# Optimization experiments

Hardware: AMD Instinct MI355X
Metric: run time of the kernel (lower is better)

## Reference

```python
import jax, jax.numpy as jnp
import numpy as np

H, KVH, HD, DM = 32, 8, 128, 4096  # attention heads, kv heads, head_dim, hidden


def _rope_tables(batch, seq, head_dim):
    # standard RoPE tables, flattened per token to match varlen layout
    inv_freq = 1.0 / (10000.0 ** (np.arange(0, head_dim, 2, dtype=np.float32) / head_dim))
    pos = np.arange(seq, dtype=np.float32)
    freqs = np.outer(pos, inv_freq)                      # [S, HD/2]
    emb = np.concatenate([freqs, freqs], axis=-1)        # [S, HD]
    cos = np.tile(np.cos(emb), (batch, 1))               # [B*S, HD]
    sin = np.tile(np.sin(emb), (batch, 1))
    return jnp.asarray(cos), jnp.asarray(sin)


def setup_inputs() -> dict:
    key = jax.random.key(0)
    k1, k2 = jax.random.split(key)
    B, S = 2, 1024
    hidden_states = jax.random.normal(k1, (B * S, DM), dtype=jnp.float32) * 0.02
    w_qkv = jax.random.normal(k2, (DM, (H + 2 * KVH) * HD), dtype=jnp.float32) * 0.02
    cos, sin = _rope_tables(B, S, HD)
    return {"hidden_states": hidden_states, "w_qkv": w_qkv, "cos": cos,
            "sin": sin, "batch_size": B, "seq_len": S}


def _rotate_half(x):
    half = x.shape[-1] // 2
    return jnp.concatenate([-x[..., half:], x[..., :half]], axis=-1)


def reference(hidden_states, w_qkv, cos, sin, batch_size, seq_len):
    B, S = batch_size, seq_len
    T = B * S
    n_rep = H // KVH
    scale = 1.0 / jnp.sqrt(jnp.asarray(HD, hidden_states.dtype))

    qkv = hidden_states @ w_qkv                           # [T, (H+2*KVH)*HD]
    q = qkv[:, : H * HD].reshape(T, H, HD)
    k = qkv[:, H * HD : (H + KVH) * HD].reshape(T, KVH, HD)
    v = qkv[:, (H + KVH) * HD :].reshape(T, KVH, HD)

    # RoPE (rotary half) on q and k
    c, s = cos[:, None, :], sin[:, None, :]
    q = q * c + _rotate_half(q) * s
    k = k * c + _rotate_half(k) * s

    # prefill SDPA branch: reshape to [B, heads, S, HD], GQA repeat on kv heads
    q = q.reshape(B, S, H, HD).transpose(0, 2, 1, 3)      # [B,H,S,HD]
    k = k.reshape(B, S, KVH, HD).transpose(0, 2, 1, 3)
    v = v.reshape(B, S, KVH, HD).transpose(0, 2, 1, 3)
    k = jnp.repeat(k, n_rep, axis=1)                      # [B,H,S,HD]
    v = jnp.repeat(v, n_rep, axis=1)

    scores = jnp.einsum("bhqd,bhkd->bhqk", q, k) * scale  # [B,H,S,S]
    causal = jnp.tril(jnp.ones((S, S), dtype=bool))
    scores = jnp.where(causal, scores, jnp.asarray(-jnp.inf, scores.dtype))
    probs = jax.nn.softmax(scores, axis=-1)
    attn = jnp.einsum("bhqk,bhkd->bhqd", probs, v)        # [B,H,S,HD]

    # postprocess_attention_output: transpose back and flatten tokens
    attn = attn.transpose(0, 2, 1, 3).reshape(T, H * HD)  # [T, H*HD]
    return attn
```

## Files before the change

kernel.cpp:

```cpp
#include <hip/hip_runtime.h>
#include <hip/hip_bf16.h>
#include <stdint.h>

constexpr int NH   = 32;
constexpr int NKVH = 8;
constexpr int HD   = 128;
constexpr int DM   = 4096;
constexpr int B    = 2;
constexpr int S    = 1024;
constexpr int T    = B * S;
constexpr int QKVN = (NH + 2 * NKVH) * HD;
constexpr int KOFF = NH * HD;
constexpr int VOFF = (NH + NKVH) * HD;

typedef float floatx4 __attribute__((ext_vector_type(4)));
typedef floatx4 floatx4_a __attribute__((may_alias));
typedef __bf16 bf16x8 __attribute__((ext_vector_type(8)));
typedef bf16x8 bf16x8_a __attribute__((may_alias));
typedef __bf16 bf16_a __attribute__((may_alias));

__device__ __forceinline__ void gload_lds16(const void* g, void* l) {
  __builtin_amdgcn_global_load_lds(
      (const __attribute__((address_space(1))) void*)g,
      (__attribute__((address_space(3))) void*)l, 16, 0, 0);
}

__global__ __launch_bounds__(256) void convert_a(const float* __restrict__ A,
                                                 __bf16* __restrict__ A16) {
  const size_t i = (size_t)(blockIdx.x * 256 + threadIdx.x) * 8;
  floatx4 v0 = *(const floatx4_a*)(A + i);
  floatx4 v1 = *(const floatx4_a*)(A + i + 4);
  bf16x8 o;
#pragma unroll
  for (int e = 0; e < 4; ++e) {
    o[e] = (__bf16)v0[e];
    o[e + 4] = (__bf16)v1[e];
  }
  *(bf16x8_a*)(A16 + i) = o;
}

__global__ __launch_bounds__(256) void transpose_w(
    const float* __restrict__ W, __bf16* __restrict__ WT) {
  __shared__ __align__(16) __bf16 ls[64][72];
  const int k0 = blockIdx.x * 64;
  const int n0 = blockIdx.y * 64;
  const int tx = threadIdx.x & 15, ty = threadIdx.x >> 4;
#pragma unroll
  for (int rr = 0; rr < 4; ++rr) {
    const int k = ty + rr * 16;
    floatx4 v = *(const floatx4_a*)(W + (size_t)(k0 + k) * QKVN + n0 + tx * 4);
#pragma unroll
    for (int e = 0; e < 4; ++e) ls[tx * 4 + e][k] = (__bf16)v[e];
  }
  __syncthreads();
#pragma unroll
  for (int it = 0; it < 2; ++it) {
    const int n = (threadIdx.x >> 3) + it * 32;
    const int c = threadIdx.x & 7;
    bf16x8 o = *(const bf16x8_a*)(&ls[n][c * 8]);
    *(bf16x8_a*)(WT + (size_t)(n0 + n) * DM + k0 + c * 8) = o;
  }
}

__global__ __launch_bounds__(256) void gemm_mfma(
    const __bf16* __restrict__ A16, const __bf16* __restrict__ W16T,
    float* __restrict__ C) {
  __shared__ __align__(16) __bf16 Asig[128 * 64];
  __shared__ __align__(16) __bf16 Bsig[128 * 64];

  const int tid = threadIdx.x;
  const int lane = tid & 63, w = tid >> 6;
  const int l15 = lane & 15, g = lane >> 4;
  const int r7 = l15 & 7;
  const int m0 = blockIdx.x * 128;
  const int n0 = blockIdx.y * 128;
  const int wrbase = (w >> 1) * 64, wcbase = (w & 1) * 64;

  const int srow = tid >> 3;
  const int sce = ((tid & 7) ^ (srow & 7)) << 3;
  const __bf16* agp = A16 + (size_t)(m0 + srow) * DM + sce;
  const __bf16* bgp = W16T + (size_t)(n0 + srow) * DM + sce;
  char* al = (char*)Asig + w * 1024;
  char* bl = (char*)Bsig + w * 1024;

  const char* Abase = (const char*)Asig + (wrbase + l15) * 128;
  const char* Bbase = (const char*)Bsig + (wcbase + l15) * 128;

  floatx4 acc[4][4];
#pragma unroll
  for (int i = 0; i < 4; ++i)
#pragma unroll
    for (int j = 0; j < 4; ++j) acc[i][j] = (floatx4){0.f, 0.f, 0.f, 0.f};

  for (int kk = 0; kk < DM; kk += 64) {
    __syncthreads();
#pragma unroll
    for (int j = 0; j < 4; ++j) {
      gload_lds16(agp + kk + (size_t)(32 * j) * DM, al + j * 4096);
      gload_lds16(bgp + kk + (size_t)(32 * j) * DM, bl + j * 4096);
    }
    __syncthreads();

#pragma unroll
    for (int kh = 0; kh < 2; ++kh) {
      const int sw = (((kh << 2) | g) ^ r7) << 4;
      bf16x8 af[4], bf[4];
#pragma unroll
      for (int i = 0; i < 4; ++i) {
        af[i] = *(const bf16x8_a*)(Abase + i * 2048 + sw);
        bf[i] = *(const bf16x8_a*)(Bbase + i * 2048 + sw);
      }
#pragma unroll
      for (int i = 0; i < 4; ++i)
#pragma unroll
        for (int j = 0; j < 4; ++j)
          acc[i][j] = __builtin_amdgcn_mfma_f32_16x16x32_bf16(af[i], bf[j],
                                                              acc[i][j], 0, 0, 0);
    }
  }

#pragma unroll
  for (int i = 0; i < 4; ++i)
#pragma unroll
    for (int j = 0; j < 4; ++j)
#pragma unroll
      for (int ri = 0; ri < 4; ++ri)
        C[(size_t)(m0 + wrbase + i * 16 + g * 4 + ri) * QKVN + n0 + wcbase +
          j * 16 + l15] = acc[i][j][ri];
}

__global__ __launch_bounds__(256) void gemm_naive(
    const float* __restrict__ A, const float* __restrict__ W,
    float* __restrict__ C) {
  __shared__ float As[16][65];
  __shared__ float Bs[16][64];
  const int tid = threadIdx.x;
  const int tx = tid & 15, ty = tid >> 4;
  const int m0 = blockIdx.y * 64, n0 = blockIdx.x * 64;
  const int sm = tid >> 2, sk4 = (tid & 3) * 4;
  const int bk = tid >> 4, bn4 = (tid & 15) * 4;
  float acc[4][4];
#pragma unroll
  for (int i = 0; i < 4; ++i)
#pragma unroll
    for (int j = 0; j < 4; ++j) acc[i][j] = 0.f;
  for (int kk = 0; kk < DM; kk += 16) {
    __syncthreads();
    floatx4 va = *(const floatx4_a*)(A + (size_t)(m0 + sm) * DM + kk + sk4);
#pragma unroll
    for (int e = 0; e < 4; ++e) As[sk4 + e][sm] = va[e];
    floatx4 vb = *(const floatx4_a*)(W + (size_t)(kk + bk) * QKVN + n0 + bn4);
    *(floatx4*)&Bs[bk][bn4] = vb;
    __syncthreads();
#pragma unroll
    for (int k = 0; k < 16; ++k) {
      float a[4], b[4];
#pragma unroll
      for (int e = 0; e < 4; ++e) a[e] = As[k][ty * 4 + e];
#pragma unroll
      for (int e = 0; e < 4; ++e) b[e] = Bs[k][tx * 4 + e];
#pragma unroll
      for (int i = 0; i < 4; ++i)
#pragma unroll
        for (int j = 0; j < 4; ++j) acc[i][j] += a[i] * b[j];
    }
  }
#pragma unroll
  for (int i = 0; i < 4; ++i)
#pragma unroll
    for (int j = 0; j < 4; ++j)
      C[(size_t)(m0 + ty * 4 + i) * QKVN + n0 + tx * 4 + j] = acc[i][j];
}

__global__ __launch_bounds__(256) void rope_kernel(
    float* __restrict__ qkv, const float* __restrict__ cs,
    const float* __restrict__ sn) {
  const int idx = blockIdx.x * 256 + threadIdx.x;
  const int d = idx & 63;
  const int tmp = idx >> 6;
  const int head = tmp % (NH + NKVH);
  const int tt = tmp / (NH + NKVH);
  float* row = qkv + (size_t)tt * QKVN + head * HD;
  const float c = cs[tt * HD + d];
  const float s = sn[tt * HD + d];
  const float x1 = row[d];
  const float x2 = row[d + 64];
  row[d] = x1 * c - x2 * s;
  row[d + 64] = x2 * c + x1 * s;
}

__global__ __launch_bounds__(256) void attn_mfma(
    const float* __restrict__ qkv, float* __restrict__ out) {
  __shared__ __align__(16) char Ksh[32 * 128 * 2];
  __shared__ __align__(16) char Vsh[128 * 32 * 2];
  __shared__ __align__(16) char Psh[4][16 * 32 * 2];

  const int tid = threadIdx.x;
  const int lane = tid & 63, wave = tid >> 6;
  const int bid = (int)blockIdx.x;
  const int qb = bid & 63;
  const int kvh = (bid >> 6) & 7;
  const int b = bid >> 9;
  const int q0 = qb * 16;
  const int h = kvh * 4 + wave;
  const int NT = (q0 + 47) >> 5;
  const float scale = 0.08838834764831845f;

  const int l15 = lane & 15, g = lane >> 4;

  bf16x8 af[4];
  {
    const float* qr = qkv + (size_t)(b * S + q0 + l15) * QKVN + h * HD;
#pragma unroll
    for (int c = 0; c < 4; ++c) {
      const int d0 = c * 32 + g * 8;
      floatx4 f0 = *(const floatx4_a*)(qr + d0);
      floatx4 f1 = *(const floatx4_a*)(qr + d0 + 4);
      bf16x8 a;
#pragma unroll
      for (int e = 0; e < 4; ++e) {
        a[e] = (__bf16)(f0[e] * scale);
        a[e + 4] = (__bf16)(f1[e] * scale);
      }
      af[c] = a;
    }
  }

  floatx4 oacc[8];
#pragma unroll
  for (int i = 0; i < 8; ++i) oacc[i] = (floatx4){0.f, 0.f, 0.f, 0.f};
  float mrow[4], lrow[4], alpha[4];
#pragma unroll
  for (int i = 0; i < 4; ++i) {
    mrow[i] = -__builtin_inff();
    lrow[i] = 0.f;
  }

  const int krow = tid >> 3, kdb = (tid & 7) * 16;
  const int vk = tid & 31, vdb = (tid >> 5) * 16;
  const float* kbaseg = qkv + (size_t)(b * S) * QKVN + KOFF + kvh * HD;
  const float* vbaseg = qkv + (size_t)(b * S) * QKVN + VOFF + kvh * HD;
  char* pb = (char*)Psh[wave];

  for (int kt = 0; kt < NT; ++kt) {
    const int kb = kt * 32;
    __syncthreads();
    {
      const float* src = kbaseg + (size_t)(kb + krow) * QKVN + kdb;
      floatx4 v0 = *(const floatx4_a*)(src);
      floatx4 v1 = *(const floatx4_a*)(src + 4);
      floatx4 v2 = *(const floatx4_a*)(src + 8);
      floatx4 v3 = *(const floatx4_a*)(src + 12);
      bf16x8 p0, p1;
#pragma unroll
      for (int e = 0; e < 4; ++e) {
        p0[e] = (__bf16)v0[e];
        p0[e + 4] = (__bf16)v1[e];
        p1[e] = (__bf16)v2[e];
        p1[e + 4] = (__bf16)v3[e];
      }
      const int swz = (krow & 7) << 4;
      const int base = krow * 256 + kdb * 2;
      *(bf16x8_a*)(Ksh + ((base) ^ swz)) = p0;
      *(bf16x8_a*)(Ksh + ((base + 16) ^ swz)) = p1;
    }
    {
      const float* src = vbaseg + (size_t)(kb + vk) * QKVN + vdb;
#pragma unroll
      for (int q4 = 0; q4 < 4; ++q4) {
        floatx4 v = *(const floatx4_a*)(src + q4 * 4);
#pragma unroll
        for (int e = 0; e < 4; ++e) {
          const int d = vdb + q4 * 4 + e;
          *(bf16_a*)(Vsh + ((d * 64 + vk * 2) ^ (((d >> 2) & 3) << 4))) =
              (__bf16)v[e];
        }
      }
    }
    __syncthreads();

    floatx4 sa0 = {0.f, 0.f, 0.f, 0.f};
    floatx4 sa1 = {0.f, 0.f, 0.f, 0.f};
    {
      const int kswz = (l15 & 7) << 4;
#pragma unroll
      for (int c = 0; c < 4; ++c) {
        bf16x8 b0 =
            *(const bf16x8_a*)(Ksh + ((l15 * 256 + c * 64 + g * 16) ^ kswz));
        bf16x8 b1 = *(const bf16x8_a*)(Ksh +
                                       (((l15 + 16) * 256 + c * 64 + g * 16) ^
                                        kswz));
        sa0 = __builtin_amdgcn_mfma_f32_16x16x32_bf16(af[c], b0, sa0, 0, 0, 0);
        sa1 = __builtin_amdgcn_mfma_f32_16x16x32_bf16(af[c], b1, sa1, 0, 0, 0);
      }
    }

    float p0a[4], p1a[4];
#pragma unroll
    for (int i = 0; i < 4; ++i) {
      const int qg = q0 + 4 * g + i;
      float s0 = sa0[i];
      float s1 = sa1[i];
      if (kb + l15 > qg) s0 = -3e38f;
      if (kb + 16 + l15 > qg) s1 = -3e38f;
      float t = fmaxf(s0, s1);
      t = fmaxf(t, __shfl_xor(t, 1));
      t = fmaxf(t, __shfl_xor(t, 2));
      t = fmaxf(t, __shfl_xor(t, 4));
      t = fmaxf(t, __shfl_xor(t, 8));
      const float mn = fmaxf(mrow[i], t);
      const float al = __expf(mrow[i] - mn);
      const float e0 = __expf(s0 - mn);
      const float e1 = __expf(s1 - mn);
      float ps = e0 + e1;
      ps += __shfl_xor(ps, 1);
      ps += __shfl_xor(ps, 2);
      ps += __shfl_xor(ps, 4);
      ps += __shfl_xor(ps, 8);
      lrow[i] = lrow[i] * al + ps;
      mrow[i] = mn;
      alpha[i] = al;
      p0a[i] = e0;
      p1a[i] = e1;
    }
#pragma unroll
    for (int df = 0; df < 8; ++df)
#pragma unroll
      for (int i = 0; i < 4; ++i) oacc[df][i] *= alpha[i];

#pragma unroll
    for (int i = 0; i < 4; ++i) {
      const int row = 4 * g + i;
      const int sw = ((row >> 1) & 3) << 4;
      *(bf16_a*)(pb + ((row * 64 + l15 * 2) ^ sw)) = (__bf16)p0a[i];
      *(bf16_a*)(pb + ((row * 64 + (16 + l15) * 2) ^ sw)) = (__bf16)p1a[i];
    }
    bf16x8 pa = *(const bf16x8_a*)(pb + ((l15 * 64 + g * 16) ^
                                         (((l15 >> 1) & 3) << 4)));

    {
      const int vswz = ((l15 >> 2) & 3) << 4;
#pragma unroll
      for (int df = 0; df < 8; ++df) {
        const int d = df * 16 + l15;
        bf16x8 vb = *(const bf16x8_a*)(Vsh + ((d * 64 + g * 16) ^ vswz));
        oacc[df] =
            __builtin_amdgcn_mfma_f32_16x16x32_bf16(pa, vb, oacc[df], 0, 0, 0);
      }
    }
  }

  float* ob = out + (size_t)(b * S + q0) * (NH * HD) + h * HD;
#pragma unroll
  for (int i = 0; i < 4; ++i) {
    const float inv = 1.f / lrow[i];
    const int row = 4 * g + i;
#pragma unroll
    for (int df = 0; df < 8; ++df)
      ob[(size_t)row * (NH * HD) + df * 16 + l15] = oacc[df][i] * inv;
  }
}

extern "C" void kernel_launch(void* const* d_in, const int* in_sizes, int n_in,
                              void* d_out, int out_size, void* d_ws,
                              size_t ws_size, hipStream_t stream) {
  const float* hidden = (const float*)d_in[0];
  const float* w_qkv = (const float*)d_in[1];
  const float* cosb = (const float*)d_in[2];
  const float* sinb = (const float*)d_in[3];
  float* out = (float*)d_out;

  char* ws = (char*)d_ws;
  float* qkv = (float*)ws;
  const size_t qkv_bytes = (size_t)T * QKVN * 4;
  const size_t wt_bytes = (size_t)QKVN * DM * 2;
  const size_t a16_bytes = (size_t)T * DM * 2;

  if (ws_size >= qkv_bytes + wt_bytes + a16_bytes) {
    __bf16* W16T = (__bf16*)(ws + qkv_bytes);
    __bf16* A16 = (__bf16*)(ws + qkv_bytes + wt_bytes);
    convert_a<<<(T * DM) / (256 * 8), 256, 0, stream>>>(hidden, A16);
    transpose_w<<<dim3(DM / 64, QKVN / 64), 256, 0, stream>>>(w_qkv, W16T);
    gemm_mfma<<<dim3(T / 128, QKVN / 128), 256, 0, stream>>>(A16, W16T, qkv);
  } else {
    gemm_naive<<<dim3(QKVN / 64, T / 64), 256, 0, stream>>>(hidden, w_qkv,
                                                            qkv);
  }
  rope_kernel<<<(T * (NH + NKVH) * 64) / 256, 256, 0, stream>>>(qkv, cosb,
                                                                sinb);
  attn_mfma<<<dim3(B * NKVH * (S / 16)), 256, 0, stream>>>(qkv, out);
}
```

Measured before the change: 470.9 us.

## Fuse RoPE into attention loads and balance causal block ordering

Removes the standalone RoPE kernel and applies rotary embedding on the fly when Q fragments and K tiles are loaded inside the attention kernel, reading cos/sin tables directly. This eliminates a full read-modify-write pass over Q and K in global memory and one kernel launch. K rotation is now recomputed for every query block that loads a tile, adding extra loads and FLOPs. The query-block index is also reversed for alternate block groups to spread causal workload more evenly across the grid.

```diff
diff --git a/kernel.cpp b/kernel.cpp
--- a/kernel.cpp
+++ b/kernel.cpp
@@ -172,35 +172,20 @@
       C[(size_t)(m0 + ty * 4 + i) * QKVN + n0 + tx * 4 + j] = acc[i][j];
 }
 
-__global__ __launch_bounds__(256) void rope_kernel(
-    float* __restrict__ qkv, const float* __restrict__ cs,
-    const float* __restrict__ sn) {
-  const int idx = blockIdx.x * 256 + threadIdx.x;
-  const int d = idx & 63;
-  const int tmp = idx >> 6;
-  const int head = tmp % (NH + NKVH);
-  const int tt = tmp / (NH + NKVH);
-  float* row = qkv + (size_t)tt * QKVN + head * HD;
-  const float c = cs[tt * HD + d];
-  const float s = sn[tt * HD + d];
-  const float x1 = row[d];
-  const float x2 = row[d + 64];
-  row[d] = x1 * c - x2 * s;
-  row[d + 64] = x2 * c + x1 * s;
-}
-
 __global__ __launch_bounds__(256) void attn_mfma(
-    const float* __restrict__ qkv, float* __restrict__ out) {
+    const float* __restrict__ qkv, const float* __restrict__ cosp,
+    const float* __restrict__ sinp, float* __restrict__ out) {
   __shared__ __align__(16) char Ksh[32 * 128 * 2];
   __shared__ __align__(16) char Vsh[128 * 32 * 2];
   __shared__ __align__(16) char Psh[4][16 * 32 * 2];
 
   const int tid = threadIdx.x;
   const int lane = tid & 63, wave = tid >> 6;
-  const int bid = (int)blockIdx.x;
-  const int qb = bid & 63;
-  const int kvh = (bid >> 6) & 7;
-  const int b = bid >> 9;
+  const int raw = (int)blockIdx.x;
+  const int qb_raw = raw & 63;
+  const int qb = ((raw >> 8) & 1) ? (63 - qb_raw) : qb_raw;
+  const int kvh = (raw >> 6) & 7;
+  const int b = raw >> 9;
   const int q0 = qb * 16;
   const int h = kvh * 4 + wave;
   const int NT = (q0 + 47) >> 5;
@@ -210,19 +195,31 @@
 
   bf16x8 af[4];
   {
-    const float* qr = qkv + (size_t)(b * S + q0 + l15) * QKVN + h * HD;
-#pragma unroll
-    for (int c = 0; c < 4; ++c) {
+    const size_t tok = (size_t)(b * S + q0 + l15);
+    const float* qr = qkv + tok * QKVN + h * HD;
+    const float* cr = cosp + tok * HD;
+    const float* sr = sinp + tok * HD;
+#pragma unroll
+    for (int c = 0; c < 2; ++c) {
       const int d0 = c * 32 + g * 8;
-      floatx4 f0 = *(const floatx4_a*)(qr + d0);
-      floatx4 f1 = *(const floatx4_a*)(qr + d0 + 4);
-      bf16x8 a;
+      floatx4 x10 = *(const floatx4_a*)(qr + d0);
+      floatx4 x11 = *(const floatx4_a*)(qr + d0 + 4);
+      floatx4 x20 = *(const floatx4_a*)(qr + d0 + 64);
+      floatx4 x21 = *(const floatx4_a*)(qr + d0 + 68);
+      floatx4 c0 = *(const floatx4_a*)(cr + d0);
+      floatx4 c1 = *(const floatx4_a*)(cr + d0 + 4);
+      floatx4 s0 = *(const floatx4_a*)(sr + d0);
+      floatx4 s1 = *(const floatx4_a*)(sr + d0 + 4);
+      bf16x8 alo, ahi;
 #pragma unroll
       for (int e = 0; e < 4; ++e) {
-        a[e] = (__bf16)(f0[e] * scale);
-        a[e + 4] = (__bf16)(f1[e] * scale);
-      }
-      af[c] = a;
+        alo[e] = (__bf16)((x10[e] * c0[e] - x20[e] * s0[e]) * scale);
+        alo[e + 4] = (__bf16)((x11[e] * c1[e] - x21[e] * s1[e]) * scale);
+        ahi[e] = (__bf16)((x20[e] * c0[e] + x10[e] * s0[e]) * scale);
+        ahi[e + 4] = (__bf16)((x21[e] * c1[e] + x11[e] * s1[e]) * scale);
+      }
+      af[c] = alo;
+      af[c + 2] = ahi;
     }
   }
 
@@ -236,33 +233,40 @@
     lrow[i] = 0.f;
   }
 
-  const int krow = tid >> 3, kdb = (tid & 7) * 16;
+  const int krow = tid >> 3, kd8 = (tid & 7) * 8;
   const int vk = tid & 31, vdb = (tid >> 5) * 16;
-  const float* kbaseg = qkv + (size_t)(b * S) * QKVN + KOFF + kvh * HD;
-  const float* vbaseg = qkv + (size_t)(b * S) * QKVN + VOFF + kvh * HD;
+  const float* kbaseg = qkv + (size_t)b * S * QKVN + KOFF + kvh * HD;
+  const float* vbaseg = qkv + (size_t)b * S * QKVN + VOFF + kvh * HD;
   char* pb = (char*)Psh[wave];
 
   for (int kt = 0; kt < NT; ++kt) {
     const int kb = kt * 32;
     __syncthreads();
     {
-      const float* src = kbaseg + (size_t)(kb + krow) * QKVN + kdb;
-      floatx4 v0 = *(const floatx4_a*)(src);
-      floatx4 v1 = *(const floatx4_a*)(src + 4);
-      floatx4 v2 = *(const floatx4_a*)(src + 8);
-      floatx4 v3 = *(const floatx4_a*)(src + 12);
-      bf16x8 p0, p1;
+      const int t = kb + krow;
+      const float* src = kbaseg + (size_t)t * QKVN + kd8;
+      const float* crk = cosp + (size_t)(b * S + t) * HD + kd8;
+      const float* srk = sinp + (size_t)(b * S + t) * HD + kd8;
+      floatx4 x10 = *(const floatx4_a*)(src);
+      floatx4 x11 = *(const floatx4_a*)(src + 4);
+      floatx4 x20 = *(const floatx4_a*)(src + 64);
+      floatx4 x21 = *(const floatx4_a*)(src + 68);
+      floatx4 c0 = *(const floatx4_a*)(crk);
+      floatx4 c1 = *(const floatx4_a*)(crk + 4);
+      floatx4 s0 = *(const floatx4_a*)(srk);
+      floatx4 s1 = *(const floatx4_a*)(srk + 4);
+      bf16x8 plo, phi;
 #pragma unroll
       for (int e = 0; e < 4; ++e) {
-        p0[e] = (__bf16)v0[e];
-        p0[e + 4] = (__bf16)v1[e];
-        p1[e] = (__bf16)v2[e];
-        p1[e + 4] = (__bf16)v3[e];
+        plo[e] = (__bf16)(x10[e] * c0[e] - x20[e] * s0[e]);
+        plo[e + 4] = (__bf16)(x11[e] * c1[e] - x21[e] * s1[e]);
+        phi[e] = (__bf16)(x20[e] * c0[e] + x10[e] * s0[e]);
+        phi[e + 4] = (__bf16)(x21[e] * c1[e] + x11[e] * s1[e]);
       }
       const int swz = (krow & 7) << 4;
-      const int base = krow * 256 + kdb * 2;
-      *(bf16x8_a*)(Ksh + ((base) ^ swz)) = p0;
-      *(bf16x8_a*)(Ksh + ((base + 16) ^ swz)) = p1;
+      const int base = krow * 256 + kd8 * 2;
+      *(bf16x8_a*)(Ksh + (base ^ swz)) = plo;
+      *(bf16x8_a*)(Ksh + ((base + 128) ^ swz)) = phi;
     }
     {
       const float* src = vbaseg + (size_t)(kb + vk) * QKVN + vdb;
@@ -386,7 +390,6 @@
     gemm_naive<<<dim3(QKVN / 64, T / 64), 256, 0, stream>>>(hidden, w_qkv,
                                                             qkv);
   }
-  rope_kernel<<<(T * (NH + NKVH) * 64) / 256, 256, 0, stream>>>(qkv, cosb,
-                                                                sinb);
-  attn_mfma<<<dim3(B * NKVH * (S / 16)), 256, 0, stream>>>(qkv, out);
-}
+  attn_mfma<<<dim3(B * NKVH * (S / 16)), 256, 0, stream>>>(qkv, cosb, sinb,
+                                                           out);
+}
```

Result: faster. 435.1 us (-7.6%).
